# Kernel tuning notes

Hardware: AMD Instinct MI355X
Metric: run time of the kernel (lower is better)

Reference implementation:

```python
import jax, jax.numpy as jnp
import numpy as np

N_NODES = 50000
N_EDGES = 640000
D = 128
BN_EPS = 1e-5
NEG_SLOPE = 0.2  # PyG GATv2Conv default negative_slope


def setup_inputs() -> dict:
    key = jax.random.key(0)
    ks = jax.random.split(key, 8)
    s = 1.0 / np.sqrt(D)
    x = jax.random.normal(ks[0], (N_NODES, D), dtype=jnp.float32)
    edge_index = jax.random.randint(ks[1], (2, N_EDGES), 0, N_NODES, dtype=jnp.int32)
    edge_attr = jax.random.uniform(ks[2], (N_EDGES, 1), dtype=jnp.float32)
    Wl = jax.random.normal(ks[3], (D, D), dtype=jnp.float32) * s
    Wr = jax.random.normal(ks[4], (D, D), dtype=jnp.float32) * s
    We = jax.random.normal(ks[5], (1, D), dtype=jnp.float32) * s
    att = jax.random.normal(ks[6], (D,), dtype=jnp.float32) * s
    return {
        "x": x, "edge_index": edge_index, "edge_attr": edge_attr,
        "Wl": Wl, "bl": jnp.zeros((D,), jnp.float32),
        "Wr": Wr, "br": jnp.zeros((D,), jnp.float32),
        "We": We, "att": att,
        "bias_out": jnp.zeros((D,), jnp.float32),
        "bn_gamma": jnp.ones((D,), jnp.float32),
        "bn_beta": jnp.zeros((D,), jnp.float32),
    }


def _gatv2(x, edge_index, edge_attr, Wl, bl, Wr, br, We, att, bias_out):
    # GATv2Conv, heads=1, concat=True, dropout treated as eval (p=0)
    src, dst = edge_index[0], edge_index[1]
    xl = x @ Wl + bl                      # source-side transform [N, D]
    xr = x @ Wr + br                      # target-side transform [N, D]
    e = edge_attr @ We                    # edge embedding       [E, D]
    m = xl[src] + xr[dst] + e             # gather + fuse        [E, D]
    m = jax.nn.leaky_relu(m, NEG_SLOPE)
    logits = m @ att                      # per-edge score [E]
    n = x.shape[0]
    # segment softmax over destination node neighborhoods
    mx = jax.ops.segment_max(logits, dst, num_segments=n)
    ex = jnp.exp(logits - mx[dst])
    den = jax.ops.segment_sum(ex, dst, num_segments=n)
    alpha = ex / (den[dst] + 1e-16)
    out = jax.ops.segment_sum(xl[src] * alpha[:, None], dst, num_segments=n)
    return out + bias_out


def reference(x, edge_index, edge_attr, Wl, bl, Wr, br, We, att, bias_out,
              bn_gamma, bn_beta):
    h = x + _gatv2(x, edge_index, edge_attr, Wl, bl, Wr, br, We, att, bias_out)
    h = jax.nn.gelu(h, approximate=False)  # torch nn.GELU default (erf)
    # BatchNorm over node dim, training-style batch stats (biased var)
    mean = jnp.mean(h, axis=0)
    var = jnp.mean((h - mean) ** 2, axis=0)
    h = (h - mean) * jax.lax.rsqrt(var + BN_EPS) * bn_gamma + bn_beta
    return h
```

## Files before the change

kernel.cpp:

```cpp
#include <hip/hip_runtime.h>
#include <math.h>

#define D 128
#define STATS_BLOCKS 512
#define SCAN_CHUNK 256

typedef __attribute__((ext_vector_type(8))) short short8;
typedef __attribute__((ext_vector_type(4))) float f32x4;

__device__ __forceinline__ unsigned short f2bf(float f) {
    unsigned u = __float_as_uint(f);
    unsigned r = (u + 0x7fff + ((u >> 16) & 1)) >> 16;
    return (unsigned short)r;
}

__global__ __launch_bounds__(256) void pack_w_k(const float* __restrict__ Wl,
    const float* __restrict__ Wr, unsigned short* __restrict__ wpack)
{
    const int lane = threadIdx.x & 63;
    const int wv = threadIdx.x >> 6;
    const int slot = blockIdx.x * 4 + wv;
    const int ct = slot >> 2;
    const int kt = slot & 3;
    const float* W = (ct < 8) ? Wl : Wr;
    const int cb = (ct & 7) * 16 + (lane & 15);
    const int kb = kt * 32 + (lane >> 4) * 8;
    unsigned short v[8];
#pragma unroll
    for (int i = 0; i < 8; i++) v[i] = f2bf(W[(size_t)(kb + i) * D + cb]);
    *(uint4*)(wpack + ((size_t)slot << 9) + lane * 8) = *(uint4*)v;
}

__global__ __launch_bounds__(256) void gemm_mfma_k(const float* __restrict__ x,
    const unsigned short* __restrict__ wpack, const float* __restrict__ bl,
    const float* __restrict__ br, unsigned* __restrict__ xlb,
    float* __restrict__ xr, int n)
{
    const int lane = threadIdx.x & 63;
    const int wv = threadIdx.x >> 6;
    const int rt = blockIdx.x * 4 + wv;
    if (rt * 16 >= n) return;
    const int r0 = rt * 16;
    const int ra = r0 + (lane & 15);
    const int r = ra < n ? ra : n - 1;
    const int ko = (lane >> 4) * 8;

    short8 a[4];
#pragma unroll
    for (int kt = 0; kt < 4; kt++) {
        const float* px = x + (size_t)r * D + kt * 32 + ko;
        float4 lo = *(const float4*)px;
        float4 hi = *(const float4*)(px + 4);
        short8 t;
        t[0] = (short)f2bf(lo.x); t[1] = (short)f2bf(lo.y);
        t[2] = (short)f2bf(lo.z); t[3] = (short)f2bf(lo.w);
        t[4] = (short)f2bf(hi.x); t[5] = (short)f2bf(hi.y);
        t[6] = (short)f2bf(hi.z); t[7] = (short)f2bf(hi.w);
        a[kt] = t;
    }

    f32x4 acc[16];
#pragma unroll
    for (int i = 0; i < 16; i++) acc[i] = (f32x4){0.f, 0.f, 0.f, 0.f};

#pragma unroll
    for (int kt = 0; kt < 4; kt++) {
#pragma unroll
        for (int ct = 0; ct < 16; ct++) {
            short8 b = *(const short8*)(wpack + (((size_t)(ct * 4 + kt)) << 9) + lane * 8);
            acc[ct] = __builtin_amdgcn_mfma_f32_16x16x32_bf16(a[kt], b, acc[ct], 0, 0, 0);
        }
    }

    const int colb = lane & 15;
    const int rbase = r0 + (lane >> 4) * 4;
#pragma unroll
    for (int ct = 8; ct < 16; ct++) {
        const int c = (ct - 8) * 16 + colb;
        const float bb = br[c];
#pragma unroll
        for (int reg = 0; reg < 4; reg++) {
            const int row = rbase + reg;
            if (row < n) xr[(size_t)row * D + c] = acc[ct][reg] + bb;
        }
    }
#pragma unroll
    for (int ct = 0; ct < 8; ct++) {
        const int c = ct * 16 + colb;
        const float bb = bl[c];
#pragma unroll
        for (int reg = 0; reg < 4; reg++) {
            unsigned mybf = f2bf(acc[ct][reg] + bb);
            unsigned other = (unsigned)__shfl_xor((int)mybf, 1);
            if ((lane & 1) == 0) {
                const int row = rbase + reg;
                if (row < n) xlb[(size_t)row * 64 + (c >> 1)] = mybf | (other << 16);
            }
        }
    }
}

__global__ __launch_bounds__(256) void hist_k(const int* __restrict__ ei,
    int* __restrict__ deg, int E)
{
    int e = blockIdx.x * blockDim.x + threadIdx.x;
    if (e < E) atomicAdd(&deg[ei[E + e]], 1);
}

__global__ __launch_bounds__(256) void scan_sum_k(const int* __restrict__ deg,
    int* __restrict__ bsum, int n)
{
    const int t = threadIdx.x;
    const int i = blockIdx.x * SCAN_CHUNK + t;
    int s = (i < n) ? deg[i] : 0;
#pragma unroll
    for (int off = 32; off > 0; off >>= 1) s += __shfl_xor(s, off);
    __shared__ int ws_[4];
    const int lane = t & 63, w = t >> 6;
    if (lane == 0) ws_[w] = s;
    __syncthreads();
    if (t == 0) bsum[blockIdx.x] = ws_[0] + ws_[1] + ws_[2] + ws_[3];
}

__global__ __launch_bounds__(256) void scan_off_k(const int* __restrict__ bsum,
    int* __restrict__ boff, int* __restrict__ rowptr, int nb, int n)
{
    const int t = threadIdx.x;
    int v = (t < nb) ? bsum[t] : 0;
    const int lane = t & 63, w = t >> 6;
    int inc = v;
#pragma unroll
    for (int off = 1; off < 64; off <<= 1) {
        int u = __shfl_up(inc, off);
        if (lane >= off) inc += u;
    }
    __shared__ int wsum[4], wpre[4];
    if (lane == 63) wsum[w] = inc;
    __syncthreads();
    if (t == 0) {
        int r = 0;
#pragma unroll
        for (int j = 0; j < 4; j++) { wpre[j] = r; r += wsum[j]; }
        rowptr[n] = r;
    }
    __syncthreads();
    if (t < nb) boff[t] = inc - v + wpre[w];
}

__global__ __launch_bounds__(256) void scan_fin_k(int* __restrict__ deg,
    const int* __restrict__ boff, int* __restrict__ rowptr, int n)
{
    const int t = threadIdx.x;
    const int i = blockIdx.x * SCAN_CHUNK + t;
    int v = (i < n) ? deg[i] : 0;
    const int lane = t & 63, w = t >> 6;
    int inc = v;
#pragma unroll
    for (int off = 1; off < 64; off <<= 1) {
        int u = __shfl_up(inc, off);
        if (lane >= off) inc += u;
    }
    __shared__ int wsum[4], wpre[4];
    if (lane == 63) wsum[w] = inc;
    __syncthreads();
    if (t == 0) {
        int r = 0;
#pragma unroll
        for (int j = 0; j < 4; j++) { wpre[j] = r; r += wsum[j]; }
    }
    __syncthreads();
    if (i < n) {
        int ex = inc - v + wpre[w] + boff[blockIdx.x];
        rowptr[i] = ex;
        deg[i] = ex;
    }
}

__global__ __launch_bounds__(256) void scatter_k(const int* __restrict__ ei,
    const float* __restrict__ ea, int* __restrict__ cursor,
    uint2* __restrict__ edges, int E)
{
    int e = blockIdx.x * blockDim.x + threadIdx.x;
    if (e >= E) return;
    int dst = ei[E + e];
    int pos = atomicAdd(&cursor[dst], 1);
    edges[pos] = make_uint2((unsigned)ei[e], __float_as_uint(ea[e]));
}

__global__ __launch_bounds__(256) void agg_k(const unsigned* __restrict__ xlb,
    const float* __restrict__ xr, const int* __restrict__ rowptr,
    const uint2* __restrict__ edges, const float* __restrict__ We,
    const float* __restrict__ att, float* __restrict__ out, int n)
{
    int wave = threadIdx.x >> 6;
    int lane = threadIdx.x & 63;
    int v = blockIdx.x * 4 + wave;
    if (v >= n) return;
    int beg = rowptr[v];
    int end = rowptr[v + 1];
    int c = lane * 2;
    float2 xrv = *(const float2*)(xr + (size_t)v * D + c);
    float2 wev = *(const float2*)(We + c);
    float2 atv = *(const float2*)(att + c);

    float m = -INFINITY, s = 0.f, acc0 = 0.f, acc1 = 0.f;

    uint2 e2[4]; unsigned xb[4];
    if (beg < end) {
#pragma unroll
        for (int e = 0; e < 4; e++) {
            int jj = beg + e < end ? beg + e : end - 1;
            e2[e] = edges[jj];
            xb[e] = xlb[(size_t)e2[e].x * 64 + lane];
        }
    }
    for (int j = beg; j < end; j += 4) {
        int jn = j + 4;
        uint2 e2n[4]; unsigned xbn[4];
#pragma unroll
        for (int e = 0; e < 4; e++) {
            int jj = jn + e < end ? jn + e : end - 1;
            e2n[e] = edges[jj];
            xbn[e] = xlb[(size_t)e2n[e].x * 64 + lane];
        }

        float p[4], xv0[4], xv1[4];
#pragma unroll
        for (int e = 0; e < 4; e++) {
            float eav = __uint_as_float(e2[e].y);
            xv0[e] = __uint_as_float(xb[e] << 16);
            xv1[e] = __uint_as_float(xb[e] & 0xffff0000u);
            float m0 = xv0[e] + xrv.x + eav * wev.x;
            float m1 = xv1[e] + xrv.y + eav * wev.y;
            m0 = m0 > 0.f ? m0 : 0.2f * m0;
            m1 = m1 > 0.f ? m1 : 0.2f * m1;
            p[e] = m0 * atv.x + m1 * atv.y;
        }
#pragma unroll
        for (int off = 32; off > 0; off >>= 1) {
#pragma unroll
            for (int e = 0; e < 4; e++) p[e] += __shfl_xor(p[e], off);
        }
#pragma unroll
        for (int e = 1; e < 4; e++) if (j + e >= end) p[e] = -INFINITY;

        float pm = fmaxf(fmaxf(p[0], p[1]), fmaxf(p[2], p[3]));
        if (pm > m) {
            float sc = __expf(m - pm);
            s *= sc; acc0 *= sc; acc1 *= sc;
            m = pm;
        }
#pragma unroll
        for (int e = 0; e < 4; e++) {
            float w = __expf(p[e] - m);
            s += w;
            acc0 += w * xv0[e];
            acc1 += w * xv1[e];
        }
#pragma unroll
        for (int e = 0; e < 4; e++) { e2[e] = e2n[e]; xb[e] = xbn[e]; }
    }
    float inv = 1.f / (s + 1e-16f);
    *(float2*)(out + (size_t)v * D + c) = make_float2(acc0 * inv, acc1 * inv);
}

__global__ __launch_bounds__(256) void gelu_stats_k(const float* __restrict__ x,
    const float* __restrict__ bias, float* __restrict__ h,
    float* __restrict__ partials, int total4)
{
    const int t = threadIdx.x;
    const int c0 = (t & 31) * 4;
    const float4 bv = *(const float4*)&bias[c0];
    float sum[4] = {0.f, 0.f, 0.f, 0.f}, sq[4] = {0.f, 0.f, 0.f, 0.f};
    const int stride = gridDim.x * blockDim.x;
    for (int i4 = blockIdx.x * blockDim.x + t; i4 < total4; i4 += stride) {
        float4 g4 = ((const float4*)h)[i4];
        float4 xv = ((const float4*)x)[i4];
        float hv[4] = {xv.x + g4.x + bv.x, xv.y + g4.y + bv.y,
                       xv.z + g4.z + bv.z, xv.w + g4.w + bv.w};
        float res[4];
#pragma unroll
        for (int j = 0; j < 4; j++) {
            float ge = 0.5f * hv[j] * (1.f + erff(hv[j] * 0.70710678118654752f));
            res[j] = ge;
            sum[j] += ge;
            sq[j] += ge * ge;
        }
        ((float4*)h)[i4] = make_float4(res[0], res[1], res[2], res[3]);
    }
    __shared__ float red[8][128];
    const int slot = t >> 5;
#pragma unroll
    for (int j = 0; j < 4; j++) red[slot][c0 + j] = sum[j];
    __syncthreads();
    if (t < 128) {
        float tot = 0.f;
#pragma unroll
        for (int s2 = 0; s2 < 8; s2++) tot += red[s2][t];
        partials[(size_t)t * STATS_BLOCKS + blockIdx.x] = tot;
    }
    __syncthreads();
#pragma unroll
    for (int j = 0; j < 4; j++) red[slot][c0 + j] = sq[j];
    __syncthreads();
    if (t < 128) {
        float tot = 0.f;
#pragma unroll
        for (int s2 = 0; s2 < 8; s2++) tot += red[s2][t];
        partials[(size_t)(128 + t) * STATS_BLOCKS + blockIdx.x] = tot;
    }
}

__global__ __launch_bounds__(256) void bn_reduce_params_k(const float* __restrict__ partials,
    const float* __restrict__ gamma, const float* __restrict__ beta,
    float* __restrict__ ab, float n)
{
    const int c = blockIdx.x;
    const int t = threadIdx.x;
    float s = 0.f, q = 0.f;
    for (int b = t; b < STATS_BLOCKS; b += 256) {
        s += partials[(size_t)c * STATS_BLOCKS + b];
        q += partials[(size_t)(128 + c) * STATS_BLOCKS + b];
    }
#pragma unroll
    for (int off = 32; off > 0; off >>= 1) {
        s += __shfl_xor(s, off);
        q += __shfl_xor(q, off);
    }
    __shared__ float ss[4], qq[4];
    const int lane = t & 63, w = t >> 6;
    if (lane == 0) { ss[w] = s; qq[w] = q; }
    __syncthreads();
    if (t == 0) {
        float S = ss[0] + ss[1] + ss[2] + ss[3];
        float Q = qq[0] + qq[1] + qq[2] + qq[3];
        float mean = S / n;
        float var = Q / n - mean * mean;
        float a = rsqrtf(var + 1e-5f) * gamma[c];
        ab[c] = a;
        ab[c + 128] = beta[c] - mean * a;
    }
}

__global__ __launch_bounds__(256) void bn_apply_k(float* __restrict__ h,
    const float* __restrict__ ab, int total4)
{
    int i4 = blockIdx.x * blockDim.x + threadIdx.x;
    if (i4 >= total4) return;
    int cg = i4 & 31;
    float4 v = ((const float4*)h)[i4];
    float4 a = ((const float4*)ab)[cg];
    float4 b = ((const float4*)(ab + 128))[cg];
    ((float4*)h)[i4] = make_float4(v.x * a.x + b.x, v.y * a.y + b.y,
                                   v.z * a.z + b.z, v.w * a.w + b.w);
}

extern "C" void kernel_launch(void* const* d_in, const int* in_sizes, int n_in,
                              void* d_out, int out_size, void* d_ws, size_t ws_size,
                              hipStream_t stream)
{
    const float* x    = (const float*)d_in[0];
    const int*   ei   = (const int*)d_in[1];
    const float* ea   = (const float*)d_in[2];
    const float* Wl   = (const float*)d_in[3];
    const float* bl   = (const float*)d_in[4];
    const float* Wr   = (const float*)d_in[5];
    const float* br   = (const float*)d_in[6];
    const float* We   = (const float*)d_in[7];
    const float* att  = (const float*)d_in[8];
    const float* bias = (const float*)d_in[9];
    const float* gamma= (const float*)d_in[10];
    const float* beta = (const float*)d_in[11];
    float* out = (float*)d_out;

    const int n = in_sizes[0] / D;
    const int E = in_sizes[1] / 2;
    const int nb = (n + SCAN_CHUNK - 1) / SCAN_CHUNK;

    char* ws = (char*)d_ws;
    unsigned short* wpack = (unsigned short*)ws;
    unsigned* xlb = (unsigned*)(ws + 65536);
    float* xr = (float*)(xlb + (size_t)n * 64);
    int* deg = (int*)(xr + (size_t)n * D);
    int* rowptr = deg + n;
    uintptr_t ep = ((uintptr_t)(rowptr + n + 1) + 7) & ~(uintptr_t)7;
    uint2* edges = (uint2*)ep;
    float* partials = (float*)(edges + E);
    int* bsum = (int*)(partials + 256 * STATS_BLOCKS);
    int* boff = bsum + nb;
    float* ab = (float*)(boff + nb);

    hipMemsetAsync(deg, 0, (size_t)n * 4, stream);

    pack_w_k<<<16, 256, 0, stream>>>(Wl, Wr, wpack);
    const int nrt = (n + 15) / 16;
    gemm_mfma_k<<<(nrt + 3) / 4, 256, 0, stream>>>(x, wpack, bl, br, xlb, xr, n);
    hist_k<<<(E + 255) / 256, 256, 0, stream>>>(ei, deg, E);
    scan_sum_k<<<nb, 256, 0, stream>>>(deg, bsum, n);
    scan_off_k<<<1, 256, 0, stream>>>(bsum, boff, rowptr, nb, n);
    scan_fin_k<<<nb, 256, 0, stream>>>(deg, boff, rowptr, n);
    scatter_k<<<(E + 255) / 256, 256, 0, stream>>>(ei, ea, deg, edges, E);
    agg_k<<<(n + 3) / 4, 256, 0, stream>>>(xlb, xr, rowptr, edges, We, att, out, n);
    const int total4 = (n * D) / 4;
    gelu_stats_k<<<STATS_BLOCKS, 256, 0, stream>>>(x, bias, out, partials, total4);
    bn_reduce_params_k<<<128, 256, 0, stream>>>(partials, gamma, beta, ab, (float)n);
    bn_apply_k<<<(total4 + 255) / 256, 256, 0, stream>>>(out, ab, total4);
}
```

Measured before the change: 190.7 us.

## Split each wave into four 16-lane groups processing separate edges in agg kernel

```diff
diff --git a/kernel.cpp b/kernel.cpp
--- a/kernel.cpp
+++ b/kernel.cpp
@@ -192,76 +192,100 @@
     const uint2* __restrict__ edges, const float* __restrict__ We,
     const float* __restrict__ att, float* __restrict__ out, int n)
 {
-    int wave = threadIdx.x >> 6;
-    int lane = threadIdx.x & 63;
-    int v = blockIdx.x * 4 + wave;
+    const int wave = threadIdx.x >> 6;
+    const int lane = threadIdx.x & 63;
+    const int g = lane >> 4;
+    const int li = lane & 15;
+    const int v = blockIdx.x * 4 + wave;
     if (v >= n) return;
-    int beg = rowptr[v];
-    int end = rowptr[v + 1];
-    int c = lane * 2;
-    float2 xrv = *(const float2*)(xr + (size_t)v * D + c);
-    float2 wev = *(const float2*)(We + c);
-    float2 atv = *(const float2*)(att + c);
-
-    float m = -INFINITY, s = 0.f, acc0 = 0.f, acc1 = 0.f;
-
-    uint2 e2[4]; unsigned xb[4];
-    if (beg < end) {
-#pragma unroll
-        for (int e = 0; e < 4; e++) {
-            int jj = beg + e < end ? beg + e : end - 1;
-            e2[e] = edges[jj];
-            xb[e] = xlb[(size_t)e2[e].x * 64 + lane];
+    const int beg = rowptr[v];
+    const int end = rowptr[v + 1];
+
+    float xrv[8], wev[8], atv[8];
+    {
+        const int f0 = li * 8;
+        float4 a0 = *(const float4*)(xr + (size_t)v * D + f0);
+        float4 a1 = *(const float4*)(xr + (size_t)v * D + f0 + 4);
+        xrv[0]=a0.x; xrv[1]=a0.y; xrv[2]=a0.z; xrv[3]=a0.w;
+        xrv[4]=a1.x; xrv[5]=a1.y; xrv[6]=a1.z; xrv[7]=a1.w;
+        float4 w0 = *(const float4*)(We + f0);
+        float4 w1 = *(const float4*)(We + f0 + 4);
+        wev[0]=w0.x; wev[1]=w0.y; wev[2]=w0.z; wev[3]=w0.w;
+        wev[4]=w1.x; wev[5]=w1.y; wev[6]=w1.z; wev[7]=w1.w;
+        float4 t0 = *(const float4*)(att + f0);
+        float4 t1 = *(const float4*)(att + f0 + 4);
+        atv[0]=t0.x; atv[1]=t0.y; atv[2]=t0.z; atv[3]=t0.w;
+        atv[4]=t1.x; atv[5]=t1.y; atv[6]=t1.z; atv[7]=t1.w;
+    }
+
+    float m = -1e30f, s = 0.f;
+    float acc[8];
+#pragma unroll
+    for (int k = 0; k < 8; k++) acc[k] = 0.f;
+
+    int j = beg + g;
+    uint2 e2 = make_uint2(0u, 0u);
+    uint4 xb4 = make_uint4(0u, 0u, 0u, 0u);
+    if (j < end) {
+        e2 = edges[j];
+        xb4 = *(const uint4*)(xlb + (size_t)e2.x * 64 + li * 4);
+    }
+    while (j < end) {
+        const int jn = j + 4;
+        const int jc = jn < end ? jn : end - 1;
+        uint2 e2n = edges[jc];
+        uint4 xbn = *(const uint4*)(xlb + (size_t)e2n.x * 64 + li * 4);
+
+        const float eav = __uint_as_float(e2.y);
+        float xv[8];
+        xv[0] = __uint_as_float(xb4.x << 16); xv[1] = __uint_as_float(xb4.x & 0xffff0000u);
+        xv[2] = __uint_as_float(xb4.y << 16); xv[3] = __uint_as_float(xb4.y & 0xffff0000u);
+        xv[4] = __uint_as_float(xb4.z << 16); xv[5] = __uint_as_float(xb4.z & 0xffff0000u);
+        xv[6] = __uint_as_float(xb4.w << 16); xv[7] = __uint_as_float(xb4.w & 0xffff0000u);
+
+        float p = 0.f;
+#pragma unroll
+        for (int k = 0; k < 8; k++) {
+            float t = fmaf(eav, wev[k], xrv[k]) + xv[k];
+            t = fmaxf(t, 0.2f * t);
+            p = fmaf(t, atv[k], p);
         }
-    }
-    for (int j = beg; j < end; j += 4) {
-        int jn = j + 4;
-        uint2 e2n[4]; unsigned xbn[4];
-#pragma unroll
-        for (int e = 0; e < 4; e++) {
-            int jj = jn + e < end ? jn + e : end - 1;
-            e2n[e] = edges[jj];
-            xbn[e] = xlb[(size_t)e2n[e].x * 64 + lane];
-        }
-
-        float p[4], xv0[4], xv1[4];
-#pragma unroll
-        for (int e = 0; e < 4; e++) {
-            float eav = __uint_as_float(e2[e].y);
-            xv0[e] = __uint_as_float(xb[e] << 16);
-            xv1[e] = __uint_as_float(xb[e] & 0xffff0000u);
-            float m0 = xv0[e] + xrv.x + eav * wev.x;
-            float m1 = xv1[e] + xrv.y + eav * wev.y;
-            m0 = m0 > 0.f ? m0 : 0.2f * m0;
-            m1 = m1 > 0.f ? m1 : 0.2f * m1;
-            p[e] = m0 * atv.x + m1 * atv.y;
-        }
-#pragma unroll
-        for (int off = 32; off > 0; off >>= 1) {
-#pragma unroll
-            for (int e = 0; e < 4; e++) p[e] += __shfl_xor(p[e], off);
-        }
-#pragma unroll
-        for (int e = 1; e < 4; e++) if (j + e >= end) p[e] = -INFINITY;
-
-        float pm = fmaxf(fmaxf(p[0], p[1]), fmaxf(p[2], p[3]));
-        if (pm > m) {
-            float sc = __expf(m - pm);
-            s *= sc; acc0 *= sc; acc1 *= sc;
-            m = pm;
-        }
-#pragma unroll
-        for (int e = 0; e < 4; e++) {
-            float w = __expf(p[e] - m);
-            s += w;
-            acc0 += w * xv0[e];
-            acc1 += w * xv1[e];
-        }
-#pragma unroll
-        for (int e = 0; e < 4; e++) { e2[e] = e2n[e]; xb[e] = xbn[e]; }
-    }
-    float inv = 1.f / (s + 1e-16f);
-    *(float2*)(out + (size_t)v * D + c) = make_float2(acc0 * inv, acc1 * inv);
+#pragma unroll
+        for (int off = 8; off >= 1; off >>= 1) p += __shfl_xor(p, off);
+
+        const float pm = fmaxf(m, p);
+        const float sc = __expf(m - pm);
+        const float w  = __expf(p - pm);
+        s = s * sc + w;
+#pragma unroll
+        for (int k = 0; k < 8; k++) acc[k] = fmaf(acc[k], sc, w * xv[k]);
+        m = pm;
+
+        e2 = e2n; xb4 = xbn; j = jn;
+    }
+
+#pragma unroll
+    for (int off = 16; off <= 32; off <<= 1) {
+        const float mo = __shfl_xor(m, off);
+        const float so = __shfl_xor(s, off);
+        const float pm = fmaxf(m, mo);
+        const float sa = __expf(m - pm);
+        const float sb = __expf(mo - pm);
+        s = s * sa + so * sb;
+#pragma unroll
+        for (int k = 0; k < 8; k++)
+            acc[k] = acc[k] * sa + __shfl_xor(acc[k], off) * sb;
+        m = pm;
+    }
+
+    if (g == 0) {
+        const float inv = 1.f / (s + 1e-16f);
+        const int f0 = li * 8;
+        float4 o0 = make_float4(acc[0]*inv, acc[1]*inv, acc[2]*inv, acc[3]*inv);
+        float4 o1 = make_float4(acc[4]*inv, acc[5]*inv, acc[6]*inv, acc[7]*inv);
+        *(float4*)(out + (size_t)v * D + f0) = o0;
+        *(float4*)(out + (size_t)v * D + f0 + 4) = o1;
+    }
 }
 
 __global__ __launch_bounds__(256) void gelu_stats_k(const float* __restrict__ x,
```

Result: faster. 173.7 us (-8.9%).
